# Optimization experiments

Measured on AMD Instinct MI355X. Metric: run time of the kernel, lower is better.

Reference implementation:

```python
import jax, jax.numpy as jnp
import numpy as np

LATENT, HID = 32, 64
NODE_FEAT, EDGE_FEAT, ENERGY_DIM, STRESS_DIM = 4, 3, 2, 9
B, N, E = 256, 200000, 1500000


def _lin(key, fan_in, fan_out):
    kw, kb = jax.random.split(key)
    s = 1.0 / np.sqrt(fan_in)
    return (jax.random.uniform(kw, (fan_in, fan_out), jnp.float32, -s, s),
            jax.random.uniform(kb, (fan_out,), jnp.float32, -s, s))


def setup_inputs() -> dict:
    key = jax.random.key(0)
    ks = jax.random.split(key, 16)
    z = jax.random.normal(ks[0], (B, LATENT), jnp.float32)
    node_emb = jax.random.normal(ks[1], (N, 2 * HID), jnp.float32)
    graph_id = jnp.sort(jax.random.randint(ks[2], (N,), 0, B))
    src = jax.random.randint(ks[3], (E,), 0, N)
    dst = jax.random.randint(ks[4], (E,), 0, N)
    lp_w, lp_b = _lin(ks[5], LATENT, 2 * HID)            # latent_proj
    nep_w, nep_b = _lin(ks[6], 2 * HID, 2 * HID)          # node_emb_proj
    nd1_w, nd1_b = _lin(ks[7], 2 * HID, HID)              # node_decoder L1
    nd2_w, nd2_b = _lin(ks[8], HID, NODE_FEAT)            # node_decoder L2
    ed1_w, ed1_b = _lin(ks[9], 4 * HID, HID)              # edge_decoder L1
    ed2_w, ed2_b = _lin(ks[10], HID, EDGE_FEAT)           # edge_decoder L2
    en1_w, en1_b = _lin(ks[11], LATENT, HID)              # energy L1
    en2_w, en2_b = _lin(ks[12], HID, ENERGY_DIM)          # energy L2
    st1_w, st1_b = _lin(ks[13], LATENT, HID)              # stress L1
    st2_w, st2_b = _lin(ks[14], HID, STRESS_DIM)          # stress L2
    return dict(z=z, node_emb=node_emb, graph_id=graph_id, src=src, dst=dst,
                lp_w=lp_w, lp_b=lp_b, nep_w=nep_w, nep_b=nep_b,
                nd1_w=nd1_w, nd1_b=nd1_b, nd2_w=nd2_w, nd2_b=nd2_b,
                ed1_w=ed1_w, ed1_b=ed1_b, ed2_w=ed2_w, ed2_b=ed2_b,
                en1_w=en1_w, en1_b=en1_b, en2_w=en2_w, en2_b=en2_b,
                st1_w=st1_w, st1_b=st1_b, st2_w=st2_w, st2_b=st2_b)


def reference(z, node_emb, graph_id, src, dst,
              lp_w, lp_b, nep_w, nep_b, nd1_w, nd1_b, nd2_w, nd2_b,
              ed1_w, ed1_b, ed2_w, ed2_b, en1_w, en1_b, en2_w, en2_b,
              st1_w, st1_b, st2_w, st2_b):
    # latent_proj + per-graph broadcast (gather replaces the Python loop)
    z_proj = jax.nn.relu(z @ lp_w + lp_b)            # [B, 2H]
    z_expanded = z_proj[graph_id]                    # [N, 2H]
    # node reconstruction (dropout is identity in eval)
    nep = jax.nn.relu(node_emb @ nep_w + nep_b)      # [N, 2H]
    h = z_expanded + nep
    recon_node = jax.nn.relu(h @ nd1_w + nd1_b) @ nd2_w + nd2_b    # [N, 4]
    # edge reconstruction: gather-concat + small MLP
    edge_input = jnp.concatenate([z_expanded[src], z_expanded[dst]], axis=1)  # [E, 4H]
    recon_edge = jax.nn.relu(edge_input @ ed1_w + ed1_b) @ ed2_w + ed2_b       # [E, 3]
    # graph-level predictors
    pred_energy = jax.nn.relu(z @ en1_w + en1_b) @ en2_w + en2_b   # [B, 2]
    pred_stress = jax.nn.relu(z @ st1_w + st1_b) @ st2_w + st2_b   # [B, 9]
    return recon_node, recon_edge, pred_energy, pred_stress
```

## Files before the change

kernel.cpp:

```cpp
#include <hip/hip_runtime.h>
#include <hip/hip_bf16.h>

#define LATENT 32
#define HID 64
#define NB 256
#define NN 200000
#define NE 1500000
#define TWOH 128

#define OUT_NODE_OFF   0
#define OUT_EDGE_OFF   (NN * 4)
#define OUT_ENERGY_OFF (OUT_EDGE_OFF + NE * 3)
#define OUT_STRESS_OFF (OUT_ENERGY_OFF + NB * 2)

#define WS_ZPROJ 0
#define WS_ZC    (WS_ZPROJ + NB*TWOH)
#define WS_P1    (WS_ZC + NB*HID)
#define WS_P2    (WS_P1 + NB*HID)
#define WS_T4    (WS_P2 + NB*HID)
#define WS_W1T   (WS_T4 + NB*NB*4)
#define WS_W2T   (WS_W1T + 8192)

typedef _Float16 half8 __attribute__((ext_vector_type(8)));
typedef _Float16 half4 __attribute__((ext_vector_type(4)));
typedef float f32x4 __attribute__((ext_vector_type(4)));

#define MT 64
#define NTILES (NN / MT)
#define NODE_BLOCKS 512
#define EDGE_BLOCKS ((NE / 4 + 255) / 256)
#define SWZ(r) (((r) & 15) << 3)

__global__ void precompute_kernel(
    const float* __restrict__ z,
    const float* __restrict__ lp_w, const float* __restrict__ lp_b,
    const float* __restrict__ nd1_w,
    const float* __restrict__ ed1_w,
    const float* __restrict__ en1_w, const float* __restrict__ en1_b,
    const float* __restrict__ en2_w, const float* __restrict__ en2_b,
    const float* __restrict__ st1_w, const float* __restrict__ st1_b,
    const float* __restrict__ st2_w, const float* __restrict__ st2_b,
    const float* __restrict__ nep_w,
    float* __restrict__ z_proj, float* __restrict__ zc,
    float* __restrict__ P1, float* __restrict__ P2,
    _Float16* __restrict__ w1T, _Float16* __restrict__ w2T,
    float* __restrict__ out_energy, float* __restrict__ out_stress)
{
    const int t = threadIdx.x;

    if (blockIdx.x >= NB) {
        const int i = (blockIdx.x - NB) * 256 + t;
        if (i < TWOH * TWOH) {
            const int n = i >> 7, k = i & 127;
            w1T[i] = (_Float16)nep_w[k * TWOH + n];
        }
        if (i < HID * TWOH) {
            const int n = i >> 7, k = i & 127;
            w2T[i] = (_Float16)nd1_w[k * HID + n];
        }
        return;
    }

    const int b = blockIdx.x;
    __shared__ float zrow[LATENT];
    __shared__ float zp[TWOH];
    __shared__ float h_en[HID];
    __shared__ float h_st[HID];

    if (t < LATENT) zrow[t] = z[b * LATENT + t];
    __syncthreads();

    if (t < TWOH) {
        float a = lp_b[t];
        #pragma unroll
        for (int k = 0; k < LATENT; ++k)
            a = fmaf(zrow[k], lp_w[k * TWOH + t], a);
        a = fmaxf(a, 0.f);
        zp[t] = a;
        z_proj[b * TWOH + t] = a;
    }
    if (t < HID) {
        float ae = en1_b[t];
        float as = st1_b[t];
        #pragma unroll
        for (int k = 0; k < LATENT; ++k) {
            ae = fmaf(zrow[k], en1_w[k * HID + t], ae);
            as = fmaf(zrow[k], st1_w[k * HID + t], as);
        }
        h_en[t] = fmaxf(ae, 0.f);
        h_st[t] = fmaxf(as, 0.f);
    }
    __syncthreads();

    if (t < HID) {
        float a = 0.f, p1 = 0.f, p2 = 0.f;
        #pragma unroll 8
        for (int k = 0; k < TWOH; ++k) {
            const float zk = zp[k];
            a  = fmaf(zk, nd1_w[k * HID + t], a);
            p1 = fmaf(zk, ed1_w[k * HID + t], p1);
            p2 = fmaf(zk, ed1_w[(TWOH + k) * HID + t], p2);
        }
        zc[b * HID + t] = a;
        P1[b * HID + t] = p1;
        P2[b * HID + t] = p2;
    }
    if (t < 2) {
        float a = en2_b[t];
        #pragma unroll 8
        for (int k = 0; k < HID; ++k) a = fmaf(h_en[k], en2_w[k * 2 + t], a);
        out_energy[b * 2 + t] = a;
    }
    if (t >= 16 && t < 25) {
        const int j = t - 16;
        float a = st2_b[j];
        #pragma unroll 8
        for (int k = 0; k < HID; ++k) a = fmaf(h_st[k], st2_w[k * 9 + j], a);
        out_stress[b * 9 + j] = a;
    }
}

__global__ void edge_table_kernel(
    const float* __restrict__ P1, const float* __restrict__ P2,
    const float* __restrict__ ed1_b,
    const float* __restrict__ ed2_w, const float* __restrict__ ed2_b,
    float4* __restrict__ T4)
{
    const int gs = blockIdx.x;
    const int t  = threadIdx.x;

    __shared__ float p1s[HID];
    __shared__ float b1s[HID];
    __shared__ float w2s[HID * 3];
    __shared__ float b2s[3];

    if (t < HID) { p1s[t] = P1[gs * HID + t]; b1s[t] = ed1_b[t]; }
    if (t >= 64 && t < 64 + HID * 3) w2s[t - 64] = ed2_w[t - 64];
    if (t < 3) b2s[t] = ed2_b[t];
    __syncthreads();

    float o0 = b2s[0], o1 = b2s[1], o2 = b2s[2];
    const float* __restrict__ p2 = &P2[t * HID];
    #pragma unroll 8
    for (int k = 0; k < HID; ++k) {
        float h = fmaxf(p1s[k] + p2[k] + b1s[k], 0.f);
        o0 = fmaf(h, w2s[k * 3 + 0], o0);
        o1 = fmaf(h, w2s[k * 3 + 1], o1);
        o2 = fmaf(h, w2s[k * 3 + 2], o2);
    }
    T4[gs * NB + t] = make_float4(o0, o1, o2, 0.f);
}

__global__ __launch_bounds__(256, 2)
void node_edge_kernel(
    const float* __restrict__ node_emb,
    const int*   __restrict__ graph_id,
    const _Float16* __restrict__ w1T,
    const float* __restrict__ nep_b,
    const _Float16* __restrict__ w2T,
    const float* __restrict__ nd1_b,
    const float* __restrict__ nd2_w, const float* __restrict__ nd2_b,
    const float* __restrict__ zc,
    const int* __restrict__ src, const int* __restrict__ dst,
    const float4* __restrict__ T4,
    float* __restrict__ out_node, float* __restrict__ out_edge)
{
    const int tid = threadIdx.x;
    const int bid = blockIdx.x;

    if (bid >= NODE_BLOCKS) {
        const int e0 = ((bid - NODE_BLOCKS) * 256 + tid) * 4;
        if (e0 >= NE) return;
        const int4 s4 = *reinterpret_cast<const int4*>(&src[e0]);
        const int4 d4 = *reinterpret_cast<const int4*>(&dst[e0]);
        const int ss[4] = {s4.x, s4.y, s4.z, s4.w};
        const int dd[4] = {d4.x, d4.y, d4.z, d4.w};
        float o[12];
        #pragma unroll
        for (int j = 0; j < 4; ++j) {
            const int gs = graph_id[ss[j]];
            const int gd = graph_id[dd[j]];
            const float4 tv = T4[gs * NB + gd];
            o[j * 3 + 0] = tv.x; o[j * 3 + 1] = tv.y; o[j * 3 + 2] = tv.z;
        }
        float4* outp = reinterpret_cast<float4*>(&out_edge[(size_t)e0 * 3]);
        outp[0] = make_float4(o[0], o[1], o[2],  o[3]);
        outp[1] = make_float4(o[4], o[5], o[6],  o[7]);
        outp[2] = make_float4(o[8], o[9], o[10], o[11]);
        return;
    }

    __shared__ _Float16 embL[2][MT * TWOH];
    __shared__ _Float16 nepL[MT * TWOH];
    __shared__ float    partL[4 * MT * 4];
    __shared__ int      gidL[2][MT];

    const int wv   = tid >> 6;
    const int lane = tid & 63;
    const int lrow = lane & 15;
    const int kg   = lane >> 4;

    half8 w1A[2][4];
    half8 w2A[4];
    #pragma unroll
    for (int cht = 0; cht < 2; ++cht)
        #pragma unroll
        for (int kb = 0; kb < 4; ++kb)
            w1A[cht][kb] = *reinterpret_cast<const half8*>(
                &w1T[(wv * 32 + cht * 16 + lrow) * TWOH + kb * 32 + kg * 8]);
    #pragma unroll
    for (int kb = 0; kb < 4; ++kb)
        w2A[kb] = *reinterpret_cast<const half8*>(
            &w2T[(wv * 16 + lrow) * TWOH + kb * 32 + kg * 8]);

    f32x4 b1r[2], b2r, w3r[4];
    #pragma unroll
    for (int cht = 0; cht < 2; ++cht)
        b1r[cht] = *reinterpret_cast<const f32x4*>(&nep_b[wv * 32 + cht * 16 + kg * 4]);
    b2r = *reinterpret_cast<const f32x4*>(&nd1_b[wv * 16 + kg * 4]);
    #pragma unroll
    for (int j = 0; j < 4; ++j)
        w3r[j] = *reinterpret_cast<const f32x4*>(&nd2_w[(wv * 16 + kg * 4 + j) * 4]);
    const float b3 = nd2_b[tid & 3];

    const int r0 = tid >> 2;
    const int q0 = tid & 3;

    {
        const float4* s4 = reinterpret_cast<const float4*>(
            node_emb + (size_t)(bid * MT + r0) * TWOH);
        float4 rr[8];
        #pragma unroll
        for (int p = 0; p < 8; ++p) rr[p] = s4[q0 + 4 * p];
        #pragma unroll
        for (int p = 0; p < 8; ++p) {
            half4 h;
            h[0] = (_Float16)rr[p].x; h[1] = (_Float16)rr[p].y;
            h[2] = (_Float16)rr[p].z; h[3] = (_Float16)rr[p].w;
            const int e = r0 * TWOH + (q0 + 4 * p) * 4;
            *reinterpret_cast<half4*>(&embL[0][e ^ SWZ(r0)]) = h;
        }
        if (tid < MT) gidL[0][tid] = graph_id[bid * MT + tid];
    }
    __syncthreads();

    int cur = 0;
    for (int t = bid; t < NTILES; t += NODE_BLOCKS) {
        const int tn = t + NODE_BLOCKS;
        const bool have_next = (tn < NTILES);

        float4 rr[8];
        int gnext = 0;
        if (have_next) {
            const float4* s4 = reinterpret_cast<const float4*>(
                node_emb + (size_t)(tn * MT + r0) * TWOH);
            #pragma unroll
            for (int p = 0; p < 8; ++p) rr[p] = s4[q0 + 4 * p];
            if (tid < MT) gnext = graph_id[tn * MT + tid];
        }

        const _Float16* eb = embL[cur];

        f32x4 acc1[2][4];
        #pragma unroll
        for (int cht = 0; cht < 2; ++cht)
            #pragma unroll
            for (int nt = 0; nt < 4; ++nt)
                acc1[cht][nt] = (f32x4){0.f, 0.f, 0.f, 0.f};

        #pragma unroll
        for (int nt = 0; nt < 4; ++nt) {
            half8 eB[4];
            #pragma unroll
            for (int kb = 0; kb < 4; ++kb) {
                const int row = nt * 16 + lrow;
                const int e = row * TWOH + kb * 32 + kg * 8;
                eB[kb] = *reinterpret_cast<const half8*>(&eb[e ^ SWZ(row)]);
            }
            #pragma unroll
            for (int cht = 0; cht < 2; ++cht)
                #pragma unroll
                for (int kb = 0; kb < 4; ++kb)
                    acc1[cht][nt] = __builtin_amdgcn_mfma_f32_16x16x32_f16(
                        w1A[cht][kb], eB[kb], acc1[cht][nt], 0, 0, 0);
        }
        #pragma unroll
        for (int cht = 0; cht < 2; ++cht)
            #pragma unroll
            for (int nt = 0; nt < 4; ++nt) {
                const int node = nt * 16 + lrow;
                const int ch = wv * 32 + cht * 16 + kg * 4;
                half4 h;
                #pragma unroll
                for (int j = 0; j < 4; ++j)
                    h[j] = (_Float16)fmaxf(acc1[cht][nt][j] + b1r[cht][j], 0.f);
                *reinterpret_cast<half4*>(
                    &nepL[(node * TWOH + ch) ^ SWZ(node)]) = h;
            }
        __syncthreads();

        f32x4 acc2[4];
        #pragma unroll
        for (int nt = 0; nt < 4; ++nt) acc2[nt] = (f32x4){0.f, 0.f, 0.f, 0.f};

        #pragma unroll
        for (int nt = 0; nt < 4; ++nt) {
            half8 nB[4];
            #pragma unroll
            for (int kb = 0; kb < 4; ++kb) {
                const int row = nt * 16 + lrow;
                const int e = row * TWOH + kb * 32 + kg * 8;
                nB[kb] = *reinterpret_cast<const half8*>(&nepL[e ^ SWZ(row)]);
            }
            #pragma unroll
            for (int kb = 0; kb < 4; ++kb)
                acc2[nt] = __builtin_amdgcn_mfma_f32_16x16x32_f16(
                    w2A[kb], nB[kb], acc2[nt], 0, 0, 0);
        }

        f32x4 p[4];
        #pragma unroll
        for (int nt = 0; nt < 4; ++nt) {
            const int node = nt * 16 + lrow;
            const int g = gidL[cur][node];
            const f32x4 z4 = *reinterpret_cast<const f32x4*>(
                &zc[(size_t)g * HID + wv * 16 + kg * 4]);
            f32x4 t4;
            #pragma unroll
            for (int j = 0; j < 4; ++j)
                t4[j] = fmaxf(acc2[nt][j] + b2r[j] + z4[j], 0.f);
            f32x4 pp = t4[0] * w3r[0];
            pp += t4[1] * w3r[1];
            pp += t4[2] * w3r[2];
            pp += t4[3] * w3r[3];
            p[nt] = pp;
        }
        #pragma unroll
        for (int nt = 0; nt < 4; ++nt) {
            #pragma unroll
            for (int j = 0; j < 4; ++j) {
                p[nt][j] += __shfl_xor(p[nt][j], 16, 64);
                p[nt][j] += __shfl_xor(p[nt][j], 32, 64);
            }
        }
        if (lane < 16) {
            #pragma unroll
            for (int nt = 0; nt < 4; ++nt)
                *reinterpret_cast<f32x4*>(
                    &partL[(wv * MT + nt * 16 + lrow) * 4]) = p[nt];
        }
        __syncthreads();

        {
            const int node = r0;
            const int o    = q0;
            const int ix = node * 4 + o;
            const float s = partL[ix] + partL[256 + ix] +
                            partL[512 + ix] + partL[768 + ix] + b3;
            out_node[(size_t)(t * MT + node) * 4 + o] = s;
        }

        if (have_next) {
            #pragma unroll
            for (int p8 = 0; p8 < 8; ++p8) {
                half4 h;
                h[0] = (_Float16)rr[p8].x; h[1] = (_Float16)rr[p8].y;
                h[2] = (_Float16)rr[p8].z; h[3] = (_Float16)rr[p8].w;
                const int e = r0 * TWOH + (q0 + 4 * p8) * 4;
                *reinterpret_cast<half4*>(&embL[cur ^ 1][e ^ SWZ(r0)]) = h;
            }
            if (tid < MT) gidL[cur ^ 1][tid] = gnext;
        }
        __syncthreads();
        cur ^= 1;
    }
}

extern "C" void kernel_launch(void* const* d_in, const int* in_sizes, int n_in,
                              void* d_out, int out_size, void* d_ws, size_t ws_size,
                              hipStream_t stream)
{
    const float* z        = (const float*)d_in[0];
    const float* node_emb = (const float*)d_in[1];
    const int*   graph_id = (const int*)  d_in[2];
    const int*   src      = (const int*)  d_in[3];
    const int*   dst      = (const int*)  d_in[4];
    const float* lp_w  = (const float*)d_in[5];
    const float* lp_b  = (const float*)d_in[6];
    const float* nep_w = (const float*)d_in[7];
    const float* nep_b = (const float*)d_in[8];
    const float* nd1_w = (const float*)d_in[9];
    const float* nd1_b = (const float*)d_in[10];
    const float* nd2_w = (const float*)d_in[11];
    const float* nd2_b = (const float*)d_in[12];
    const float* ed1_w = (const float*)d_in[13];
    const float* ed1_b = (const float*)d_in[14];
    const float* ed2_w = (const float*)d_in[15];
    const float* ed2_b = (const float*)d_in[16];
    const float* en1_w = (const float*)d_in[17];
    const float* en1_b = (const float*)d_in[18];
    const float* en2_w = (const float*)d_in[19];
    const float* en2_b = (const float*)d_in[20];
    const float* st1_w = (const float*)d_in[21];
    const float* st1_b = (const float*)d_in[22];
    const float* st2_w = (const float*)d_in[23];
    const float* st2_b = (const float*)d_in[24];

    float* out = (float*)d_out;
    float* out_node   = out + OUT_NODE_OFF;
    float* out_edge   = out + OUT_EDGE_OFF;
    float* out_energy = out + OUT_ENERGY_OFF;
    float* out_stress = out + OUT_STRESS_OFF;

    float* ws     = (float*)d_ws;
    float* z_proj = ws + WS_ZPROJ;
    float* zc     = ws + WS_ZC;
    float* P1     = ws + WS_P1;
    float* P2     = ws + WS_P2;
    float4* T4    = (float4*)(ws + WS_T4);
    _Float16* w1T = (_Float16*)(ws + WS_W1T);
    _Float16* w2T = (_Float16*)(ws + WS_W2T);

    precompute_kernel<<<NB + 64, 256, 0, stream>>>(
        z, lp_w, lp_b, nd1_w, ed1_w,
        en1_w, en1_b, en2_w, en2_b, st1_w, st1_b, st2_w, st2_b, nep_w,
        z_proj, zc, P1, P2, w1T, w2T, out_energy, out_stress);

    edge_table_kernel<<<NB, NB, 0, stream>>>(P1, P2, ed1_b, ed2_w, ed2_b, T4);

    node_edge_kernel<<<NODE_BLOCKS + EDGE_BLOCKS, 256, 0, stream>>>(
        node_emb, graph_id, w1T, nep_b, w2T, nd1_b, nd2_w, nd2_b, zc,
        src, dst, T4, out_node, out_edge);
}
```

Baseline: 249.5 us.

## Replace persistent double-buffered node loop with one tile per block

The node path no longer runs 512 persistent blocks that loop over tiles with a double-buffered LDS staging of node_emb. It now launches one block per 64-node tile and loads node_emb straight from global memory into MFMA B-operand registers, converting to fp16 in registers. This drops the embL LDS buffers and a barrier per tile, and raises launch_bounds occupancy to 3 blocks per SIMD group. The edge table kernel also folds the bias into the shared P1 row and reads P2 as float4. In exchange, the weight fragments are reloaded by every block and there is no explicit prefetch overlap.

```diff
diff --git a/kernel.cpp b/kernel.cpp
--- a/kernel.cpp
+++ b/kernel.cpp
@@ -27,7 +27,6 @@
 
 #define MT 64
 #define NTILES (NN / MT)
-#define NODE_BLOCKS 512
 #define EDGE_BLOCKS ((NE / 4 + 255) / 256)
 #define SWZ(r) (((r) & 15) << 3)
 
@@ -130,28 +129,32 @@
     const int t  = threadIdx.x;
 
     __shared__ float p1s[HID];
-    __shared__ float b1s[HID];
     __shared__ float w2s[HID * 3];
     __shared__ float b2s[3];
 
-    if (t < HID) { p1s[t] = P1[gs * HID + t]; b1s[t] = ed1_b[t]; }
+    if (t < HID) p1s[t] = P1[gs * HID + t] + ed1_b[t];
     if (t >= 64 && t < 64 + HID * 3) w2s[t - 64] = ed2_w[t - 64];
     if (t < 3) b2s[t] = ed2_b[t];
     __syncthreads();
 
     float o0 = b2s[0], o1 = b2s[1], o2 = b2s[2];
-    const float* __restrict__ p2 = &P2[t * HID];
-    #pragma unroll 8
-    for (int k = 0; k < HID; ++k) {
-        float h = fmaxf(p1s[k] + p2[k] + b1s[k], 0.f);
-        o0 = fmaf(h, w2s[k * 3 + 0], o0);
-        o1 = fmaf(h, w2s[k * 3 + 1], o1);
-        o2 = fmaf(h, w2s[k * 3 + 2], o2);
+    const f32x4* __restrict__ p2 = reinterpret_cast<const f32x4*>(&P2[t * HID]);
+    #pragma unroll 4
+    for (int k4 = 0; k4 < 16; ++k4) {
+        const f32x4 pv = p2[k4];
+        #pragma unroll
+        for (int j = 0; j < 4; ++j) {
+            const int k = k4 * 4 + j;
+            const float h = fmaxf(p1s[k] + pv[j], 0.f);
+            o0 = fmaf(h, w2s[k * 3 + 0], o0);
+            o1 = fmaf(h, w2s[k * 3 + 1], o1);
+            o2 = fmaf(h, w2s[k * 3 + 2], o2);
+        }
     }
     T4[gs * NB + t] = make_float4(o0, o1, o2, 0.f);
 }
 
-__global__ __launch_bounds__(256, 2)
+__global__ __launch_bounds__(256, 3)
 void node_edge_kernel(
     const float* __restrict__ node_emb,
     const int*   __restrict__ graph_id,
@@ -168,8 +171,8 @@
     const int tid = threadIdx.x;
     const int bid = blockIdx.x;
 
-    if (bid >= NODE_BLOCKS) {
-        const int e0 = ((bid - NODE_BLOCKS) * 256 + tid) * 4;
+    if (bid >= NTILES) {
+        const int e0 = ((bid - NTILES) * 256 + tid) * 4;
         if (e0 >= NE) return;
         const int4 s4 = *reinterpret_cast<const int4*>(&src[e0]);
         const int4 d4 = *reinterpret_cast<const int4*>(&dst[e0]);
@@ -190,24 +193,26 @@
         return;
     }
 
-    __shared__ _Float16 embL[2][MT * TWOH];
     __shared__ _Float16 nepL[MT * TWOH];
     __shared__ float    partL[4 * MT * 4];
-    __shared__ int      gidL[2][MT];
+    __shared__ int      gidL[MT];
 
     const int wv   = tid >> 6;
     const int lane = tid & 63;
     const int lrow = lane & 15;
     const int kg   = lane >> 4;
+    const size_t nbase = (size_t)bid * MT;
+
+    if (tid < MT) gidL[tid] = graph_id[nbase + tid];
 
     half8 w1A[2][4];
-    half8 w2A[4];
     #pragma unroll
     for (int cht = 0; cht < 2; ++cht)
         #pragma unroll
         for (int kb = 0; kb < 4; ++kb)
             w1A[cht][kb] = *reinterpret_cast<const half8*>(
                 &w1T[(wv * 32 + cht * 16 + lrow) * TWOH + kb * 32 + kg * 8]);
+    half8 w2A[4];
     #pragma unroll
     for (int kb = 0; kb < 4; ++kb)
         w2A[kb] = *reinterpret_cast<const half8*>(
@@ -223,156 +228,105 @@
         w3r[j] = *reinterpret_cast<const f32x4*>(&nd2_w[(wv * 16 + kg * 4 + j) * 4]);
     const float b3 = nd2_b[tid & 3];
 
-    const int r0 = tid >> 2;
-    const int q0 = tid & 3;
-
-    {
-        const float4* s4 = reinterpret_cast<const float4*>(
-            node_emb + (size_t)(bid * MT + r0) * TWOH);
-        float4 rr[8];
-        #pragma unroll
-        for (int p = 0; p < 8; ++p) rr[p] = s4[q0 + 4 * p];
-        #pragma unroll
-        for (int p = 0; p < 8; ++p) {
-            half4 h;
-            h[0] = (_Float16)rr[p].x; h[1] = (_Float16)rr[p].y;
-            h[2] = (_Float16)rr[p].z; h[3] = (_Float16)rr[p].w;
-            const int e = r0 * TWOH + (q0 + 4 * p) * 4;
-            *reinterpret_cast<half4*>(&embL[0][e ^ SWZ(r0)]) = h;
-        }
-        if (tid < MT) gidL[0][tid] = graph_id[bid * MT + tid];
-    }
-    __syncthreads();
-
-    int cur = 0;
-    for (int t = bid; t < NTILES; t += NODE_BLOCKS) {
-        const int tn = t + NODE_BLOCKS;
-        const bool have_next = (tn < NTILES);
-
-        float4 rr[8];
-        int gnext = 0;
-        if (have_next) {
-            const float4* s4 = reinterpret_cast<const float4*>(
-                node_emb + (size_t)(tn * MT + r0) * TWOH);
-            #pragma unroll
-            for (int p = 0; p < 8; ++p) rr[p] = s4[q0 + 4 * p];
-            if (tid < MT) gnext = graph_id[tn * MT + tid];
-        }
-
-        const _Float16* eb = embL[cur];
-
-        f32x4 acc1[2][4];
-        #pragma unroll
-        for (int cht = 0; cht < 2; ++cht)
-            #pragma unroll
-            for (int nt = 0; nt < 4; ++nt)
-                acc1[cht][nt] = (f32x4){0.f, 0.f, 0.f, 0.f};
-
-        #pragma unroll
-        for (int nt = 0; nt < 4; ++nt) {
-            half8 eB[4];
-            #pragma unroll
-            for (int kb = 0; kb < 4; ++kb) {
-                const int row = nt * 16 + lrow;
-                const int e = row * TWOH + kb * 32 + kg * 8;
-                eB[kb] = *reinterpret_cast<const half8*>(&eb[e ^ SWZ(row)]);
-            }
-            #pragma unroll
-            for (int cht = 0; cht < 2; ++cht)
-                #pragma unroll
-                for (int kb = 0; kb < 4; ++kb)
-                    acc1[cht][nt] = __builtin_amdgcn_mfma_f32_16x16x32_f16(
-                        w1A[cht][kb], eB[kb], acc1[cht][nt], 0, 0, 0);
-        }
-        #pragma unroll
-        for (int cht = 0; cht < 2; ++cht)
-            #pragma unroll
-            for (int nt = 0; nt < 4; ++nt) {
-                const int node = nt * 16 + lrow;
-                const int ch = wv * 32 + cht * 16 + kg * 4;
-                half4 h;
-                #pragma unroll
-                for (int j = 0; j < 4; ++j)
-                    h[j] = (_Float16)fmaxf(acc1[cht][nt][j] + b1r[cht][j], 0.f);
-                *reinterpret_cast<half4*>(
-                    &nepL[(node * TWOH + ch) ^ SWZ(node)]) = h;
-            }
-        __syncthreads();
-
-        f32x4 acc2[4];
-        #pragma unroll
-        for (int nt = 0; nt < 4; ++nt) acc2[nt] = (f32x4){0.f, 0.f, 0.f, 0.f};
-
-        #pragma unroll
-        for (int nt = 0; nt < 4; ++nt) {
-            half8 nB[4];
-            #pragma unroll
-            for (int kb = 0; kb < 4; ++kb) {
-                const int row = nt * 16 + lrow;
-                const int e = row * TWOH + kb * 32 + kg * 8;
-                nB[kb] = *reinterpret_cast<const half8*>(&nepL[e ^ SWZ(row)]);
-            }
-            #pragma unroll
-            for (int kb = 0; kb < 4; ++kb)
-                acc2[nt] = __builtin_amdgcn_mfma_f32_16x16x32_f16(
-                    w2A[kb], nB[kb], acc2[nt], 0, 0, 0);
-        }
-
-        f32x4 p[4];
+    f32x4 acc1[2][4];
+    #pragma unroll
+    for (int cht = 0; cht < 2; ++cht)
+        #pragma unroll
+        for (int nt = 0; nt < 4; ++nt)
+            acc1[cht][nt] = (f32x4){0.f, 0.f, 0.f, 0.f};
+
+    #pragma unroll
+    for (int nt = 0; nt < 4; ++nt) {
+        const float* ep = node_emb + (nbase + nt * 16 + lrow) * TWOH + kg * 8;
+        f32x4 u[4], v[4];
+        #pragma unroll
+        for (int kb = 0; kb < 4; ++kb) {
+            u[kb] = *reinterpret_cast<const f32x4*>(ep + kb * 32);
+            v[kb] = *reinterpret_cast<const f32x4*>(ep + kb * 32 + 4);
+        }
+        #pragma unroll
+        for (int kb = 0; kb < 4; ++kb) {
+            half8 h;
+            h[0] = (_Float16)u[kb][0]; h[1] = (_Float16)u[kb][1];
+            h[2] = (_Float16)u[kb][2]; h[3] = (_Float16)u[kb][3];
+            h[4] = (_Float16)v[kb][0]; h[5] = (_Float16)v[kb][1];
+            h[6] = (_Float16)v[kb][2]; h[7] = (_Float16)v[kb][3];
+            acc1[0][nt] = __builtin_amdgcn_mfma_f32_16x16x32_f16(
+                w1A[0][kb], h, acc1[0][nt], 0, 0, 0);
+            acc1[1][nt] = __builtin_amdgcn_mfma_f32_16x16x32_f16(
+                w1A[1][kb], h, acc1[1][nt], 0, 0, 0);
+        }
+    }
+    #pragma unroll
+    for (int cht = 0; cht < 2; ++cht)
         #pragma unroll
         for (int nt = 0; nt < 4; ++nt) {
             const int node = nt * 16 + lrow;
-            const int g = gidL[cur][node];
-            const f32x4 z4 = *reinterpret_cast<const f32x4*>(
-                &zc[(size_t)g * HID + wv * 16 + kg * 4]);
-            f32x4 t4;
+            const int ch = wv * 32 + cht * 16 + kg * 4;
+            half4 h;
             #pragma unroll
             for (int j = 0; j < 4; ++j)
-                t4[j] = fmaxf(acc2[nt][j] + b2r[j] + z4[j], 0.f);
-            f32x4 pp = t4[0] * w3r[0];
-            pp += t4[1] * w3r[1];
-            pp += t4[2] * w3r[2];
-            pp += t4[3] * w3r[3];
-            p[nt] = pp;
-        }
-        #pragma unroll
-        for (int nt = 0; nt < 4; ++nt) {
-            #pragma unroll
-            for (int j = 0; j < 4; ++j) {
-                p[nt][j] += __shfl_xor(p[nt][j], 16, 64);
-                p[nt][j] += __shfl_xor(p[nt][j], 32, 64);
-            }
-        }
-        if (lane < 16) {
-            #pragma unroll
-            for (int nt = 0; nt < 4; ++nt)
-                *reinterpret_cast<f32x4*>(
-                    &partL[(wv * MT + nt * 16 + lrow) * 4]) = p[nt];
-        }
-        __syncthreads();
-
-        {
-            const int node = r0;
-            const int o    = q0;
-            const int ix = node * 4 + o;
-            const float s = partL[ix] + partL[256 + ix] +
-                            partL[512 + ix] + partL[768 + ix] + b3;
-            out_node[(size_t)(t * MT + node) * 4 + o] = s;
-        }
-
-        if (have_next) {
-            #pragma unroll
-            for (int p8 = 0; p8 < 8; ++p8) {
-                half4 h;
-                h[0] = (_Float16)rr[p8].x; h[1] = (_Float16)rr[p8].y;
-                h[2] = (_Float16)rr[p8].z; h[3] = (_Float16)rr[p8].w;
-                const int e = r0 * TWOH + (q0 + 4 * p8) * 4;
-                *reinterpret_cast<half4*>(&embL[cur ^ 1][e ^ SWZ(r0)]) = h;
-            }
-            if (tid < MT) gidL[cur ^ 1][tid] = gnext;
-        }
-        __syncthreads();
-        cur ^= 1;
+                h[j] = (_Float16)fmaxf(acc1[cht][nt][j] + b1r[cht][j], 0.f);
+            *reinterpret_cast<half4*>(&nepL[(node * TWOH + ch) ^ SWZ(node)]) = h;
+        }
+    __syncthreads();
+
+    f32x4 acc2[4];
+    #pragma unroll
+    for (int nt = 0; nt < 4; ++nt) acc2[nt] = (f32x4){0.f, 0.f, 0.f, 0.f};
+
+    #pragma unroll
+    for (int nt = 0; nt < 4; ++nt) {
+        #pragma unroll
+        for (int kb = 0; kb < 4; ++kb) {
+            const int node = nt * 16 + lrow;
+            const int e = node * TWOH + kb * 32 + kg * 8;
+            const half8 nB = *reinterpret_cast<const half8*>(&nepL[e ^ SWZ(node)]);
+            acc2[nt] = __builtin_amdgcn_mfma_f32_16x16x32_f16(
+                w2A[kb], nB, acc2[nt], 0, 0, 0);
+        }
+    }
+
+    f32x4 p[4];
+    #pragma unroll
+    for (int nt = 0; nt < 4; ++nt) {
+        const int node = nt * 16 + lrow;
+        const int g = gidL[node];
+        const f32x4 z4 = *reinterpret_cast<const f32x4*>(
+            &zc[(size_t)g * HID + wv * 16 + kg * 4]);
+        f32x4 t4;
+        #pragma unroll
+        for (int j = 0; j < 4; ++j)
+            t4[j] = fmaxf(acc2[nt][j] + b2r[j] + z4[j], 0.f);
+        f32x4 pp = t4[0] * w3r[0];
+        pp += t4[1] * w3r[1];
+        pp += t4[2] * w3r[2];
+        pp += t4[3] * w3r[3];
+        p[nt] = pp;
+    }
+    #pragma unroll
+    for (int nt = 0; nt < 4; ++nt) {
+        #pragma unroll
+        for (int j = 0; j < 4; ++j) {
+            p[nt][j] += __shfl_xor(p[nt][j], 16, 64);
+            p[nt][j] += __shfl_xor(p[nt][j], 32, 64);
+        }
+    }
+    if (lane < 16) {
+        #pragma unroll
+        for (int nt = 0; nt < 4; ++nt)
+            *reinterpret_cast<f32x4*>(
+                &partL[(wv * MT + nt * 16 + lrow) * 4]) = p[nt];
+    }
+    __syncthreads();
+
+    {
+        const int node = tid >> 2;
+        const int o    = tid & 3;
+        const int ix = node * 4 + o;
+        const float s = partL[ix] + partL[256 + ix] +
+                        partL[512 + ix] + partL[768 + ix] + b3;
+        out_node[(nbase + node) * 4 + o] = s;
     }
 }
 
@@ -428,7 +382,7 @@
 
     edge_table_kernel<<<NB, NB, 0, stream>>>(P1, P2, ed1_b, ed2_w, ed2_b, T4);
 
-    node_edge_kernel<<<NODE_BLOCKS + EDGE_BLOCKS, 256, 0, stream>>>(
+    node_edge_kernel<<<NTILES + EDGE_BLOCKS, 256, 0, stream>>>(
         node_emb, graph_id, w1T, nep_b, w2T, nd1_b, nd2_w, nd2_b, zc,
         src, dst, T4, out_node, out_edge);
 }
```

Measured after the change: 282.1 us. 1.13x slower.
